# Kernel optimization log

Hardware: AMD Instinct MI355X
Metric: run time of the kernel (lower is better)

## Reference

```python
import jax, jax.numpy as jnp
import numpy as np

N_NODES = 100000


def _add_self_loops(edge_index, n):
    loop = jnp.arange(n, dtype=edge_index.dtype)
    src = jnp.concatenate([edge_index[0], loop])
    dst = jnp.concatenate([edge_index[1], loop])
    return src, dst


def _gcn_norm(src, dst, n):
    # PyG gcn_norm: degree over dst (col), norm = d^-1/2[src] * d^-1/2[dst]
    deg = jax.ops.segment_sum(jnp.ones_like(dst, dtype=jnp.float32), dst, num_segments=n)
    dinv = jnp.where(deg > 0, jax.lax.rsqrt(jnp.maximum(deg, 1.0)), 0.0)
    return dinv[src] * dinv[dst]


def _gcn_conv(x, W, b, src, dst, norm, n):
    h = x @ W                              # [N, out]
    msg = h[src] * norm[:, None]           # gather + scale  [E', out]
    out = jax.ops.segment_sum(msg, dst, num_segments=n)  # scatter-add
    if b is not None:
        out = out + b
    return out


def setup_inputs() -> dict:
    key = jax.random.key(0)
    ks = jax.random.split(key, 8)
    n, e = N_NODES, 1600000
    in_d, hid, out_d, L = 128, 64, 64, 3
    x = jax.random.normal(ks[0], (n, in_d), dtype=jnp.float32)
    edge_index = jax.random.randint(ks[1], (2, e), 0, n, dtype=jnp.int64)
    s = lambda fan_in: 1.0 / np.sqrt(fan_in)
    W_in = jax.random.normal(ks[2], (in_d, hid), dtype=jnp.float32) * s(in_d)
    b_in = jnp.zeros((hid,), dtype=jnp.float32)
    W_h = jax.random.normal(ks[3], (L, hid, hid), dtype=jnp.float32) * s(hid)
    b_h = jnp.zeros((L, hid), dtype=jnp.float32)
    W_out = jax.random.normal(ks[4], (hid, out_d), dtype=jnp.float32) * s(hid)
    return {"x": x, "edge_index": edge_index, "W_in": W_in, "b_in": b_in,
            "W_h": W_h, "b_h": b_h, "W_out": W_out}


def reference(x, edge_index, W_in, b_in, W_h, b_h, W_out):
    n = x.shape[0]
    src, dst = _add_self_loops(edge_index, n)
    norm = _gcn_norm(src, dst, n)
    h = _gcn_conv(x, W_in, b_in, src, dst, norm, n)
    for i in range(W_h.shape[0]):
        h = _gcn_conv(h, W_h[i], b_h[i], src, dst, norm, n)
        h = jax.nn.relu(h)
    return _gcn_conv(h, W_out, None, src, dst, norm, n)
```

## Files before the change

### kernel.cpp

```cpp
#include <hip/hip_runtime.h>
#include <hip/hip_fp16.h>

#define HID 64
#define BIN_SHIFT 9
#define BIN_SIZE  512
#define SC_TILE   8192


typedef _Float16 f16x8 __attribute__((ext_vector_type(8)));
typedef float    f32x4 __attribute__((ext_vector_type(4)));

__global__ void zero_i(int* __restrict__ p, int n) {
    int i = blockIdx.x * 256 + threadIdx.x, st = gridDim.x * 256;
    for (; i < n; i += st) p[i] = 0;
}

__global__ void dinv_k(const int* __restrict__ deg, float* __restrict__ dinv, int N) {
    int i = blockIdx.x * 256 + threadIdx.x;
    if (i < N) dinv[i] = rsqrtf((float)deg[i] + 1.0f);
}

__global__ void wfrag_prep(const float* __restrict__ W_in, const float* __restrict__ W_h,
                           const float* __restrict__ W_out, __half* __restrict__ wfrag) {
    int s = blockIdx.x, l = threadIdx.x;
    const float* W; int base, ls;
    if (s < 16)      { W = W_in;                      base = 0;                ls = s; }
    else if (s < 40) { int t = s - 16; int L = t >> 3;
                       W = W_h + (size_t)L * 64 * 64; base = 1024 + L * 512;   ls = t & 7; }
    else             { W = W_out;                     base = 2560;             ls = s - 40; }
    int ks = ls >> 2, ct = ls & 3;
    int col = ct * 16 + (l & 15);
    int k0  = ks * 32 + (l >> 4) * 8;
    __half v[8];
    #pragma unroll
    for (int j = 0; j < 8; ++j) v[j] = __float2half_rn(W[(size_t)(k0 + j) * HID + col]);
    *(uint4*)&wfrag[(size_t)(base + ls * 64 + l) * 8] = *(uint4*)v;
}

template<bool IN32, int NKS>
__global__ __launch_bounds__(256)
void gemm_mfma(const void* __restrict__ Hin, const __half* __restrict__ wfl,
               const float* __restrict__ dinv, __half* __restrict__ out, int N) {
    const int l  = threadIdx.x & 63;
    const int wv = threadIdx.x >> 6;
    const int rA = l & 15;
    const int gK = l >> 4;
    const int rb = blockIdx.x * 128 + wv * 32;

    f16x8 bf[NKS][4];
    #pragma unroll
    for (int ks = 0; ks < NKS; ++ks)
        #pragma unroll
        for (int ct = 0; ct < 4; ++ct)
            bf[ks][ct] = *(const f16x8*)(wfl + (size_t)((ks * 4 + ct) * 64 + l) * 8);

    f16x8 af[NKS][2];
    #pragma unroll
    for (int rt = 0; rt < 2; ++rt) {
        int r = rb + rt * 16 + rA; if (r > N - 1) r = N - 1;
        if (IN32) {
            const float* H = (const float*)Hin;
            const float* p = H + (size_t)r * (NKS * 32) + gK * 8;
            #pragma unroll
            for (int ks = 0; ks < NKS; ++ks) {
                f32x4 a = *(const f32x4*)(p + ks * 32);
                f32x4 b = *(const f32x4*)(p + ks * 32 + 4);
                f16x8 t;
                t[0] = (_Float16)a[0]; t[1] = (_Float16)a[1];
                t[2] = (_Float16)a[2]; t[3] = (_Float16)a[3];
                t[4] = (_Float16)b[0]; t[5] = (_Float16)b[1];
                t[6] = (_Float16)b[2]; t[7] = (_Float16)b[3];
                af[ks][rt] = t;
            }
        } else {
            const __half* H = (const __half*)Hin;
            #pragma unroll
            for (int ks = 0; ks < NKS; ++ks)
                af[ks][rt] = *(const f16x8*)(H + (size_t)r * HID + ks * 32 + gK * 8);
        }
    }

    f32x4 acc[2][4];
    #pragma unroll
    for (int rt = 0; rt < 2; ++rt)
        #pragma unroll
        for (int ct = 0; ct < 4; ++ct)
            acc[rt][ct] = (f32x4){0.f, 0.f, 0.f, 0.f};

    #pragma unroll
    for (int ks = 0; ks < NKS; ++ks)
        #pragma unroll
        for (int rt = 0; rt < 2; ++rt)
            #pragma unroll
            for (int ct = 0; ct < 4; ++ct)
                acc[rt][ct] = __builtin_amdgcn_mfma_f32_16x16x32_f16(
                    af[ks][rt], bf[ks][ct], acc[rt][ct], 0, 0, 0);

    #pragma unroll
    for (int rt = 0; rt < 2; ++rt) {
        int r0 = rb + rt * 16 + gK * 4;
        float dv[4];
        #pragma unroll
        for (int j = 0; j < 4; ++j) dv[j] = dinv[min(r0 + j, N - 1)];
        #pragma unroll
        for (int ct = 0; ct < 4; ++ct)
            #pragma unroll
            for (int j = 0; j < 4; ++j) {
                int r = r0 + j;
                if (r < N)
                    out[(size_t)r * HID + ct * 16 + rA] =
                        __float2half_rn(acc[rt][ct][j] * dv[j]);
            }
    }
}

__global__ void bin_count(const int* __restrict__ dst, int* __restrict__ binCount,
                          int E, int nbins) {
    __shared__ int c[1024];
    for (int i = threadIdx.x; i < nbins; i += 256) c[i] = 0;
    __syncthreads();
    int chunk = (E + gridDim.x - 1) / gridDim.x;
    int s0 = blockIdx.x * chunk, s1 = min(E, s0 + chunk);
    for (int e = s0 + threadIdx.x; e < s1; e += 256)
        atomicAdd(&c[dst[e] >> BIN_SHIFT], 1);
    __syncthreads();
    for (int i = threadIdx.x; i < nbins; i += 256)
        if (c[i]) atomicAdd(&binCount[i], c[i]);
}

__global__ void bin_scan(const int* __restrict__ binCount, int* __restrict__ binOff,
                         int* __restrict__ binCursor, int nb, int E) {
    __shared__ int s[256];
    int t = threadIdx.x, base = t * 4;
    int v0 = 0, v1 = 0, v2 = 0, v3 = 0;
    if (base + 0 < nb) v0 = binCount[base + 0];
    if (base + 1 < nb) v1 = binCount[base + 1];
    if (base + 2 < nb) v2 = binCount[base + 2];
    if (base + 3 < nb) v3 = binCount[base + 3];
    int sum = v0 + v1 + v2 + v3;
    s[t] = sum; __syncthreads();
    for (int off = 1; off < 256; off <<= 1) {
        int x = (t >= off) ? s[t - off] : 0;
        __syncthreads(); s[t] += x; __syncthreads();
    }
    int run = s[t] - sum;
    if (base + 0 < nb) { binOff[base + 0] = run; binCursor[base + 0] = run; } run += v0;
    if (base + 1 < nb) { binOff[base + 1] = run; binCursor[base + 1] = run; } run += v1;
    if (base + 2 < nb) { binOff[base + 2] = run; binCursor[base + 2] = run; } run += v2;
    if (base + 3 < nb) { binOff[base + 3] = run; binCursor[base + 3] = run; } run += v3;
    if (t == 0) binOff[nb] = E;
}

__global__ void bin_scatter(const int* __restrict__ src, const int* __restrict__ dst,
                            int* __restrict__ binCursor, unsigned* __restrict__ packed,
                            int E, int nbins) {
    __shared__ int cnt[1024];
    __shared__ int cur[1024];
    int t = threadIdx.x;
    int s0 = blockIdx.x * SC_TILE, s1 = min(E, s0 + SC_TILE);
    for (int i = t; i < nbins; i += 256) cnt[i] = 0;
    __syncthreads();
    for (int e = s0 + t; e < s1; e += 256)
        atomicAdd(&cnt[dst[e] >> BIN_SHIFT], 1);
    __syncthreads();
    for (int b = t; b < nbins; b += 256)
        cur[b] = cnt[b] ? atomicAdd(&binCursor[b], cnt[b]) : 0;
    __syncthreads();
    for (int e = s0 + t; e < s1; e += 256) {
        int d = dst[e];
        int b = d >> BIN_SHIFT;
        int pos = atomicAdd(&cur[b], 1);
        packed[pos] = ((unsigned)src[e] << BIN_SHIFT) | (unsigned)(d & (BIN_SIZE - 1));
    }
}

__global__ void csr_count(const unsigned* __restrict__ packed, const int* __restrict__ binOff,
                          int* __restrict__ deg, int N) {
    __shared__ int c[BIN_SIZE];
    int t = threadIdx.x, b = blockIdx.x;
    for (int i = t; i < BIN_SIZE; i += 256) c[i] = 0;
    int j0 = binOff[b], j1 = binOff[b + 1];
    __syncthreads();
    for (int j = j0 + t; j < j1; j += 256)
        atomicAdd(&c[packed[j] & (BIN_SIZE - 1)], 1);
    __syncthreads();
    int base = b << BIN_SHIFT;
    for (int i = t; i < BIN_SIZE; i += 256) {
        int nd = base + i;
        if (nd < N) deg[nd] = c[i];
    }
}

__global__ void csr_scatter(const unsigned* __restrict__ packed, const int* __restrict__ binOff,
                            const int* __restrict__ rp, int* __restrict__ esrc, int N) {
    __shared__ int cur[BIN_SIZE];
    __shared__ int rps[BIN_SIZE];
    int t = threadIdx.x, b = blockIdx.x;
    int base = b << BIN_SHIFT;
    for (int i = t; i < BIN_SIZE; i += 256) {
        cur[i] = 0;
        int nd = base + i;
        rps[i] = (nd < N) ? rp[nd] : 0;
    }
    int j0 = binOff[b], j1 = binOff[b + 1];
    __syncthreads();
    for (int j = j0 + t; j < j1; j += 256) {
        unsigned p = packed[j];
        int dl = p & (BIN_SIZE - 1);
        int pos = rps[dl] + atomicAdd(&cur[dl], 1);
        esrc[pos] = (int)(p >> BIN_SHIFT);
    }
}

__global__ void scan1(const int* __restrict__ in, int* __restrict__ out,
                      int* __restrict__ bsum, int n) {
    __shared__ int s[256];
    int t = threadIdx.x, base = blockIdx.x * 1024 + t * 4;
    int v0 = 0, v1 = 0, v2 = 0, v3 = 0;
    if (base + 0 < n) v0 = in[base + 0];
    if (base + 1 < n) v1 = in[base + 1];
    if (base + 2 < n) v2 = in[base + 2];
    if (base + 3 < n) v3 = in[base + 3];
    int sum = v0 + v1 + v2 + v3;
    s[t] = sum; __syncthreads();
    for (int off = 1; off < 256; off <<= 1) {
        int x = (t >= off) ? s[t - off] : 0;
        __syncthreads(); s[t] += x; __syncthreads();
    }
    if (t == 255) bsum[blockIdx.x] = s[255];
    int run = s[t] - sum;
    if (base + 0 < n) out[base + 0] = run; run += v0;
    if (base + 1 < n) out[base + 1] = run; run += v1;
    if (base + 2 < n) out[base + 2] = run; run += v2;
    if (base + 3 < n) out[base + 3] = run;
}

__global__ void scan2(int* __restrict__ bsum, int nb) {
    __shared__ int s[256];
    int t = threadIdx.x, base = t * 4;
    int v0 = 0, v1 = 0, v2 = 0, v3 = 0;
    if (base + 0 < nb) v0 = bsum[base + 0];
    if (base + 1 < nb) v1 = bsum[base + 1];
    if (base + 2 < nb) v2 = bsum[base + 2];
    if (base + 3 < nb) v3 = bsum[base + 3];
    int sum = v0 + v1 + v2 + v3;
    s[t] = sum; __syncthreads();
    for (int off = 1; off < 256; off <<= 1) {
        int x = (t >= off) ? s[t - off] : 0;
        __syncthreads(); s[t] += x; __syncthreads();
    }
    int run = s[t] - sum;
    if (base + 0 < nb) bsum[base + 0] = run; run += v0;
    if (base + 1 < nb) bsum[base + 1] = run; run += v1;
    if (base + 2 < nb) bsum[base + 2] = run; run += v2;
    if (base + 3 < nb) bsum[base + 3] = run;
}

__global__ void scan3(int* __restrict__ out, const int* __restrict__ bsum,
                      int n, int N, int E) {
    int i = blockIdx.x * 256 + threadIdx.x;
    if (i < n) out[i] += bsum[i >> 10];
    if (i == 0) out[N] = E;
}

__global__ void agg_csr(const __half* __restrict__ tmp, const int* __restrict__ rp,
                        const int* __restrict__ esrc, const float* __restrict__ dinv,
                        const float* __restrict__ bias, float* __restrict__ outf,
                        __half* __restrict__ houtp, int N, int do_relu) {
    const int wave = threadIdx.x >> 6;
    const int lane = threadIdx.x & 63;
    const int g    = lane & 7;
    const int sub  = lane >> 3;
    const int stride = gridDim.x * 4;

    int d = blockIdx.x * 4 + wave;
    if (d >= N) return;
    int j0 = rp[d], j1 = rp[d + 1];
    int sp = (j0 + lane < j1) ? esrc[j0 + lane] : 0;

    while (d < N) {
        const int dn = d + stride;
        int nj0 = 0, nj1 = 0;
        if (dn < N) { nj0 = rp[dn]; nj1 = rp[dn + 1]; }

        uint4 vself = make_uint4(0, 0, 0, 0);
        if (sub == 0) vself = ((const uint4*)(tmp + (size_t)d * HID))[g];
        float acc[8];
        {
            const __half2* h2 = (const __half2*)&vself;
            #pragma unroll
            for (int i = 0; i < 4; ++i) {
                float2 f = __half22float2(h2[i]);
                acc[2 * i]     = f.x;
                acc[2 * i + 1] = f.y;
            }
        }

        int cs = sp, base = j0;
        while (base < j1) {
            int cnt = min(64, j1 - base);
            int jj = 0;
            for (; jj + 16 <= cnt; jj += 16) {
                int s0 = __shfl(cs, jj + sub);
                int s1 = __shfl(cs, jj + 8 + sub);
                uint4 v0 = ((const uint4*)(tmp + (size_t)s0 * HID))[g];
                uint4 v1 = ((const uint4*)(tmp + (size_t)s1 * HID))[g];
                const __half2* h0 = (const __half2*)&v0;
                const __half2* h1 = (const __half2*)&v1;
                #pragma unroll
                for (int i = 0; i < 4; ++i) {
                    float2 f0 = __half22float2(h0[i]);
                    float2 f1 = __half22float2(h1[i]);
                    acc[2 * i]     += f0.x + f1.x;
                    acc[2 * i + 1] += f0.y + f1.y;
                }
            }
            if (jj + 8 <= cnt) {
                int s0 = __shfl(cs, jj + sub);
                uint4 v0 = ((const uint4*)(tmp + (size_t)s0 * HID))[g];
                const __half2* h0 = (const __half2*)&v0;
                #pragma unroll
                for (int i = 0; i < 4; ++i) {
                    float2 f = __half22float2(h0[i]);
                    acc[2 * i] += f.x; acc[2 * i + 1] += f.y;
                }
                jj += 8;
            }
            if (jj < cnt) {
                int e = jj + sub;
                int s0 = __shfl(cs, min(e, cnt - 1));
                if (e < cnt) {
                    uint4 v = ((const uint4*)(tmp + (size_t)s0 * HID))[g];
                    const __half2* h2 = (const __half2*)&v;
                    #pragma unroll
                    for (int i = 0; i < 4; ++i) {
                        float2 f = __half22float2(h2[i]);
                        acc[2 * i] += f.x; acc[2 * i + 1] += f.y;
                    }
                }
            }
            base += 64;
            if (base < j1) {
                int rem = j1 - base;
                cs = (lane < rem) ? esrc[base + lane] : 0;
            }
        }

        int nsp = 0;
        if (dn < N) nsp = (nj0 + lane < nj1) ? esrc[nj0 + lane] : 0;

        #pragma unroll
        for (int i = 0; i < 8; ++i) {
            float a = acc[i];
            a += __shfl_xor(a, 8);
            a += __shfl_xor(a, 16);
            a += __shfl_xor(a, 32);
            acc[i] = a;
        }
        if (sub == 0) {
            float di = dinv[d];
            float o[8];
            #pragma unroll
            for (int i = 0; i < 8; ++i) o[i] = di * acc[i];
            if (bias != nullptr) {
                #pragma unroll
                for (int i = 0; i < 8; ++i) o[i] += bias[g * 8 + i];
            }
            if (do_relu) {
                #pragma unroll
                for (int i = 0; i < 8; ++i) o[i] = fmaxf(o[i], 0.0f);
            }
            if (houtp != nullptr) {
                __half2 ph[4];
                #pragma unroll
                for (int i = 0; i < 4; ++i)
                    ph[i] = __halves2half2(__float2half_rn(o[2 * i]),
                                           __float2half_rn(o[2 * i + 1]));
                *(uint4*)&houtp[(size_t)d * HID + g * 8] = *(uint4*)ph;
            } else {
                float* orow = &outf[(size_t)d * HID + g * 8];
                *(float4*)orow       = make_float4(o[0], o[1], o[2], o[3]);
                *(float4*)(orow + 4) = make_float4(o[4], o[5], o[6], o[7]);
            }
        }
        d = dn; j0 = nj0; j1 = nj1; sp = nsp;
    }
}

extern "C" void kernel_launch(void* const* d_in, const int* in_sizes, int n_in,
                              void* d_out, int out_size, void* d_ws, size_t ws_size,
                              hipStream_t stream) {
    const float* x     = (const float*)d_in[0];
    const int*   ei    = (const int*)d_in[1];
    const float* W_in  = (const float*)d_in[2];
    const float* b_in  = (const float*)d_in[3];
    const float* W_h   = (const float*)d_in[4];
    const float* b_h   = (const float*)d_in[5];
    const float* W_out = (const float*)d_in[6];

    const int K0 = in_sizes[2] / HID;
    const int N  = in_sizes[0] / K0;
    const int E  = in_sizes[1] / 2;
    const int* srcp = ei;
    const int* dstp = ei + E;

    const int NH = N * HID;
    const size_t Npad = ((size_t)N + 255) & ~(size_t)255;
    const int nbins = (N + BIN_SIZE - 1) >> BIN_SHIFT;

    float*  ACC = (float*)d_out;
    __half* h16 = (__half*)d_out;

    float*    dinv   = (float*)d_ws;
    __half*   tmp    = (__half*)(dinv + Npad);
    unsigned* packed = (unsigned*)tmp;
    int*      degi   = (int*)(tmp + NH);
    int*      rp     = degi + Npad;
    int*      bsum   = rp + Npad + 256;
    int*      esrc   = bsum + 1024;
    int*      binCount  = esrc + E;
    int*      binOff    = binCount + 1024;
    int*      binCursor = binOff + 1026;
    uintptr_t wf_addr = (uintptr_t)(binCursor + 1024);
    wf_addr = (wf_addr + 15) & ~(uintptr_t)15;
    __half*   wfrag  = (__half*)wf_addr;

    const int tgrid = (N + 127) / 128;
    const int agrid = 2048;
    const int nb    = (N + 1023) / 1024;
    const int sgrid = (E + SC_TILE - 1) / SC_TILE;

    wfrag_prep<<<48, 64, 0, stream>>>(W_in, W_h, W_out, wfrag);
    zero_i<<<1, 256, 0, stream>>>(binCount, nbins);
    bin_count<<<nbins, 256, 0, stream>>>(dstp, binCount, E, nbins);
    bin_scan<<<1, 256, 0, stream>>>(binCount, binOff, binCursor, nbins, E);
    bin_scatter<<<sgrid, 256, 0, stream>>>(srcp, dstp, binCursor, packed, E, nbins);
    csr_count<<<nbins, 256, 0, stream>>>(packed, binOff, degi, N);
    dinv_k<<<(N + 255) / 256, 256, 0, stream>>>(degi, dinv, N);
    scan1<<<nb, 256, 0, stream>>>(degi, rp, bsum, N);
    scan2<<<1, 256, 0, stream>>>(bsum, nb);
    scan3<<<(N + 255) / 256, 256, 0, stream>>>(rp, bsum, N, N, E);
    csr_scatter<<<nbins, 256, 0, stream>>>(packed, binOff, rp, esrc, N);

    gemm_mfma<true, 4><<<tgrid, 256, 0, stream>>>(x, wfrag, dinv, tmp, N);
    agg_csr<<<agrid, 256, 0, stream>>>(tmp, rp, esrc, dinv, b_in, nullptr, h16, N, 0);
    for (int l = 0; l < 3; ++l) {
        gemm_mfma<false, 2><<<tgrid, 256, 0, stream>>>(
            h16, wfrag + (size_t)(1024 + l * 512) * 8, dinv, tmp, N);
        agg_csr<<<agrid, 256, 0, stream>>>(tmp, rp, esrc, dinv, b_h + (size_t)l * HID,
                                           nullptr, h16, N, 1);
    }
    gemm_mfma<false, 2><<<tgrid, 256, 0, stream>>>(
        h16, wfrag + (size_t)2560 * 8, dinv, tmp, N);
    agg_csr<<<agrid, 256, 0, stream>>>(tmp, rp, esrc, dinv, nullptr, ACC, nullptr, N, 0);
}
```

Before: 442.2 us.

## Fuse CSR count, scan, dinv and scatter into one per-bin kernel

Replaces csr_count, dinv_k, the three-kernel global scan and csr_scatter with one csr_build kernel per destination bin. Each block computes per-node degrees in shared memory and scans them locally, offset by the bin's global start. It then writes rp and dinv and scatters esrc using shared-memory cursors. This cuts five launches and the global degree/rowptr round trips. bin_count's grid also changes from nbins to a fixed 784 blocks.

```diff
diff --git a/kernel.cpp b/kernel.cpp
--- a/kernel.cpp
+++ b/kernel.cpp
@@ -13,11 +13,6 @@
 __global__ void zero_i(int* __restrict__ p, int n) {
     int i = blockIdx.x * 256 + threadIdx.x, st = gridDim.x * 256;
     for (; i < n; i += st) p[i] = 0;
-}
-
-__global__ void dinv_k(const int* __restrict__ deg, float* __restrict__ dinv, int N) {
-    int i = blockIdx.x * 256 + threadIdx.x;
-    if (i < N) dinv[i] = rsqrtf((float)deg[i] + 1.0f);
 }
 
 __global__ void wfrag_prep(const float* __restrict__ W_in, const float* __restrict__ W_h,
@@ -174,93 +169,48 @@
     }
 }
 
-__global__ void csr_count(const unsigned* __restrict__ packed, const int* __restrict__ binOff,
-                          int* __restrict__ deg, int N) {
+__global__ void csr_build(const unsigned* __restrict__ packed, const int* __restrict__ binOff,
+                          int* __restrict__ rp, int* __restrict__ esrc,
+                          float* __restrict__ dinv, int N, int E) {
     __shared__ int c[BIN_SIZE];
+    __shared__ int off[BIN_SIZE];
     int t = threadIdx.x, b = blockIdx.x;
-    for (int i = t; i < BIN_SIZE; i += 256) c[i] = 0;
+    int i0 = t, i1 = t + 256;
+    c[i0] = 0; c[i1] = 0;
+    __syncthreads();
     int j0 = binOff[b], j1 = binOff[b + 1];
-    __syncthreads();
     for (int j = j0 + t; j < j1; j += 256)
         atomicAdd(&c[packed[j] & (BIN_SIZE - 1)], 1);
     __syncthreads();
+    off[i0] = c[i0]; off[i1] = c[i1];
+    __syncthreads();
+    for (int o = 1; o < BIN_SIZE; o <<= 1) {
+        int v0 = (i0 >= o) ? off[i0 - o] : 0;
+        int v1 = (i1 >= o) ? off[i1 - o] : 0;
+        __syncthreads();
+        off[i0] += v0; off[i1] += v1;
+        __syncthreads();
+    }
     int base = b << BIN_SHIFT;
-    for (int i = t; i < BIN_SIZE; i += 256) {
+    #pragma unroll
+    for (int q = 0; q < 2; ++q) {
+        int i  = t + q * 256;
         int nd = base + i;
-        if (nd < N) deg[nd] = c[i];
-    }
-}
-
-__global__ void csr_scatter(const unsigned* __restrict__ packed, const int* __restrict__ binOff,
-                            const int* __restrict__ rp, int* __restrict__ esrc, int N) {
-    __shared__ int cur[BIN_SIZE];
-    __shared__ int rps[BIN_SIZE];
-    int t = threadIdx.x, b = blockIdx.x;
-    int base = b << BIN_SHIFT;
-    for (int i = t; i < BIN_SIZE; i += 256) {
-        cur[i] = 0;
-        int nd = base + i;
-        rps[i] = (nd < N) ? rp[nd] : 0;
-    }
-    int j0 = binOff[b], j1 = binOff[b + 1];
+        int excl = off[i] - c[i];
+        if (nd < N) {
+            rp[nd]   = j0 + excl;
+            dinv[nd] = rsqrtf((float)c[i] + 1.0f);
+        }
+        c[i] = j0 + excl;
+    }
+    if (b == 0 && t == 0) rp[N] = E;
     __syncthreads();
     for (int j = j0 + t; j < j1; j += 256) {
         unsigned p = packed[j];
         int dl = p & (BIN_SIZE - 1);
-        int pos = rps[dl] + atomicAdd(&cur[dl], 1);
+        int pos = atomicAdd(&c[dl], 1);
         esrc[pos] = (int)(p >> BIN_SHIFT);
     }
-}
-
-__global__ void scan1(const int* __restrict__ in, int* __restrict__ out,
-                      int* __restrict__ bsum, int n) {
-    __shared__ int s[256];
-    int t = threadIdx.x, base = blockIdx.x * 1024 + t * 4;
-    int v0 = 0, v1 = 0, v2 = 0, v3 = 0;
-    if (base + 0 < n) v0 = in[base + 0];
-    if (base + 1 < n) v1 = in[base + 1];
-    if (base + 2 < n) v2 = in[base + 2];
-    if (base + 3 < n) v3 = in[base + 3];
-    int sum = v0 + v1 + v2 + v3;
-    s[t] = sum; __syncthreads();
-    for (int off = 1; off < 256; off <<= 1) {
-        int x = (t >= off) ? s[t - off] : 0;
-        __syncthreads(); s[t] += x; __syncthreads();
-    }
-    if (t == 255) bsum[blockIdx.x] = s[255];
-    int run = s[t] - sum;
-    if (base + 0 < n) out[base + 0] = run; run += v0;
-    if (base + 1 < n) out[base + 1] = run; run += v1;
-    if (base + 2 < n) out[base + 2] = run; run += v2;
-    if (base + 3 < n) out[base + 3] = run;
-}
-
-__global__ void scan2(int* __restrict__ bsum, int nb) {
-    __shared__ int s[256];
-    int t = threadIdx.x, base = t * 4;
-    int v0 = 0, v1 = 0, v2 = 0, v3 = 0;
-    if (base + 0 < nb) v0 = bsum[base + 0];
-    if (base + 1 < nb) v1 = bsum[base + 1];
-    if (base + 2 < nb) v2 = bsum[base + 2];
-    if (base + 3 < nb) v3 = bsum[base + 3];
-    int sum = v0 + v1 + v2 + v3;
-    s[t] = sum; __syncthreads();
-    for (int off = 1; off < 256; off <<= 1) {
-        int x = (t >= off) ? s[t - off] : 0;
-        __syncthreads(); s[t] += x; __syncthreads();
-    }
-    int run = s[t] - sum;
-    if (base + 0 < nb) bsum[base + 0] = run; run += v0;
-    if (base + 1 < nb) bsum[base + 1] = run; run += v1;
-    if (base + 2 < nb) bsum[base + 2] = run; run += v2;
-    if (base + 3 < nb) bsum[base + 3] = run;
-}
-
-__global__ void scan3(int* __restrict__ out, const int* __restrict__ bsum,
-                      int n, int N, int E) {
-    int i = blockIdx.x * 256 + threadIdx.x;
-    if (i < n) out[i] += bsum[i >> 10];
-    if (i == 0) out[N] = E;
 }
 
 __global__ void agg_csr(const __half* __restrict__ tmp, const int* __restrict__ rp,
@@ -414,10 +364,8 @@
     float*    dinv   = (float*)d_ws;
     __half*   tmp    = (__half*)(dinv + Npad);
     unsigned* packed = (unsigned*)tmp;
-    int*      degi   = (int*)(tmp + NH);
-    int*      rp     = degi + Npad;
-    int*      bsum   = rp + Npad + 256;
-    int*      esrc   = bsum + 1024;
+    int*      rp     = (int*)(tmp + NH);
+    int*      esrc   = rp + Npad + 256;
     int*      binCount  = esrc + E;
     int*      binOff    = binCount + 1024;
     int*      binCursor = binOff + 1026;
@@ -427,20 +375,14 @@
 
     const int tgrid = (N + 127) / 128;
     const int agrid = 2048;
-    const int nb    = (N + 1023) / 1024;
     const int sgrid = (E + SC_TILE - 1) / SC_TILE;
 
     wfrag_prep<<<48, 64, 0, stream>>>(W_in, W_h, W_out, wfrag);
     zero_i<<<1, 256, 0, stream>>>(binCount, nbins);
-    bin_count<<<nbins, 256, 0, stream>>>(dstp, binCount, E, nbins);
+    bin_count<<<784, 256, 0, stream>>>(dstp, binCount, E, nbins);
     bin_scan<<<1, 256, 0, stream>>>(binCount, binOff, binCursor, nbins, E);
     bin_scatter<<<sgrid, 256, 0, stream>>>(srcp, dstp, binCursor, packed, E, nbins);
-    csr_count<<<nbins, 256, 0, stream>>>(packed, binOff, degi, N);
-    dinv_k<<<(N + 255) / 256, 256, 0, stream>>>(degi, dinv, N);
-    scan1<<<nb, 256, 0, stream>>>(degi, rp, bsum, N);
-    scan2<<<1, 256, 0, stream>>>(bsum, nb);
-    scan3<<<(N + 255) / 256, 256, 0, stream>>>(rp, bsum, N, N, E);
-    csr_scatter<<<nbins, 256, 0, stream>>>(packed, binOff, rp, esrc, N);
+    csr_build<<<nbins, 256, 0, stream>>>(packed, binOff, rp, esrc, dinv, N, E);
 
     gemm_mfma<true, 4><<<tgrid, 256, 0, stream>>>(x, wfrag, dinv, tmp, N);
     agg_csr<<<agrid, 256, 0, stream>>>(tmp, rp, esrc, dinv, b_in, nullptr, h16, N, 0);
```

After: 440.7 us. Within noise of the previous version (-0.3%).
